# Kernel tuning notes

Measured on AMD Instinct MI355X. Metric: run time of the kernel, lower is better.

## Reference

```python
import jax, jax.numpy as jnp
import numpy as np

SEQ_LEN = 9
HALF = SEQ_LEN // 2  # padding = 4
EPS = 1e-5


def _bn(x, g, b, m, v):
    # BatchNorm1d in eval mode (running stats); dropout disabled (eval).
    return g * (x - m) * jax.lax.rsqrt(v + EPS) + b


def _segment_avgpool(x, segment_key):
    """Per-consecutive-segment AvgPool1d(k=9, stride=1, pad=4, count_include_pad=False).

    x: [B, D] features ordered in time, segment_key: [B] consecutive segment ids.
    Vectorized: windows never cross segment boundaries, so a global prefix sum
    plus per-frame clamped window bounds reproduces the per-segment pooling.
    """
    B, D = x.shape
    idx = jnp.arange(B)
    changed = segment_key[1:] != segment_key[:-1]
    is_start = jnp.concatenate([jnp.array([True]), changed])
    is_end = jnp.concatenate([changed, jnp.array([True])])
    seg_start = jax.lax.cummax(jnp.where(is_start, idx, 0), axis=0)
    seg_end = jax.lax.cummin(jnp.where(is_end, idx, B - 1), axis=0, reverse=True)
    lo = jnp.maximum(idx - HALF, seg_start)
    hi = jnp.minimum(idx + HALF, seg_end)
    csum = jnp.concatenate([jnp.zeros((1, D), x.dtype), jnp.cumsum(x, axis=0)], axis=0)  # [B+1, D]
    sums = csum[hi + 1] - csum[lo]
    counts = (hi - lo + 1).astype(x.dtype)  # count_include_pad=False
    return sums / counts[:, None]


def setup_inputs() -> dict:
    key = jax.random.key(0)
    ks = jax.random.split(key, 16)
    B, F, D3, H = 16384, 2048, 600, 2048
    n_seg = 200
    inp = {
        'img_feat': jax.random.normal(ks[0], (B, F), jnp.float32),
        'segment_key': jnp.sort(jax.random.randint(ks[1], (B,), 0, n_seg, jnp.int32)),
        # to_3d linear
        'W3d': jax.random.normal(ks[2], (D3, F), jnp.float32) * (1.0 / np.sqrt(F)),
        'b3d': jax.random.normal(ks[3], (D3,), jnp.float32) * 0.01,
        # block 1 (bef_pool): Linear(D3->H) + ReLU + BN
        'W1': jax.random.normal(ks[4], (H, D3), jnp.float32) * (1.0 / np.sqrt(D3)),
        'b1': jax.random.normal(ks[5], (H,), jnp.float32) * 0.01,
        'g1': jnp.ones((H,), jnp.float32),
        'be1': jnp.zeros((H,), jnp.float32),
        'm1': jax.random.normal(ks[6], (H,), jnp.float32) * 0.1,
        'v1': jax.random.uniform(ks[7], (H,), jnp.float32, 0.5, 1.5),
        # block 2 (pain head): Linear(H->H) + ReLU + BN
        'W2': jax.random.normal(ks[8], (H, H), jnp.float32) * (1.0 / np.sqrt(H)),
        'b2': jax.random.normal(ks[9], (H,), jnp.float32) * 0.01,
        'g2': jnp.ones((H,), jnp.float32),
        'be2': jnp.zeros((H,), jnp.float32),
        'm2': jax.random.normal(ks[10], (H,), jnp.float32) * 0.1,
        'v2': jax.random.uniform(ks[11], (H,), jnp.float32, 0.5, 1.5),
        # final pain linear H -> 2
        'Wp': jax.random.normal(ks[12], (2, H), jnp.float32) * (1.0 / np.sqrt(H)),
        'bp': jax.random.normal(ks[13], (2,), jnp.float32) * 0.01,
    }
    return inp


def reference(img_feat, segment_key, W3d, b3d, W1, b1, g1, be1, m1, v1,
              W2, b2, g2, be2, m2, v2, Wp, bp):
    latent_3d = img_feat @ W3d.T + b3d                       # [B, D3]
    h = _bn(jax.nn.relu(latent_3d @ W1.T + b1), g1, be1, m1, v1)  # bef_pool, [B, H]
    pooled = _segment_avgpool(h, segment_key)                # ragged windowed avg
    h2 = _bn(jax.nn.relu(pooled @ W2.T + b2), g2, be2, m2, v2)
    output_pain = h2 @ Wp.T + bp                             # [B, 2]
    pain_pred = jax.nn.softmax(output_pain, axis=1)
    return output_pain, pain_pred
```

## Files before the change

kernel.cpp:

```cpp
#include <hip/hip_runtime.h>
#include <hip/hip_bf16.h>
#include <math.h>
#include <stdint.h>

#define DEVI static __device__ __forceinline__

typedef __attribute__((ext_vector_type(8))) short short8;
typedef __attribute__((ext_vector_type(4))) float f32x4;
typedef __attribute__((ext_vector_type(4))) float float4v;
typedef __attribute__((ext_vector_type(4))) unsigned short ushort4v;
typedef __attribute__((ext_vector_type(8))) unsigned short ushort8;

DEVI unsigned short f2bf(float f) {
  unsigned int u = __builtin_bit_cast(unsigned int, f);
  u += 0x7fffu + ((u >> 16) & 1u);
  return (unsigned short)(u >> 16);
}
DEVI float bf2f(unsigned short s) {
  unsigned int u = ((unsigned int)s) << 16;
  return __builtin_bit_cast(float, u);
}

DEVI void gl_lds16(const unsigned short* g, unsigned short* l) {
  __builtin_amdgcn_global_load_lds(
      (const __attribute__((address_space(1))) void*)g,
      (__attribute__((address_space(3))) void*)l, 16, 0, 0);
}

__global__ __launch_bounds__(256) void cast_pad(const float* __restrict__ src,
                                                unsigned short* __restrict__ dst,
                                                int srcR, int srcC, int dstR, int dstC) {
  size_t n4 = (size_t)dstR * (size_t)dstC / 4;
  for (size_t i = (size_t)blockIdx.x * blockDim.x + threadIdx.x; i < n4;
       i += (size_t)gridDim.x * blockDim.x) {
    size_t e = i * 4;
    int r = (int)(e / (size_t)dstC);
    int c = (int)(e % (size_t)dstC);
    float4v v;
    if (r < srcR && c + 3 < srcC) {
      v = *(const float4v*)(src + (size_t)r * srcC + c);
    } else {
#pragma unroll
      for (int j = 0; j < 4; ++j) {
        int cc = c + j;
        v[j] = (r < srcR && cc < srcC) ? src[(size_t)r * srcC + cc] : 0.f;
      }
    }
    ushort4v o;
#pragma unroll
    for (int j = 0; j < 4; ++j) o[j] = f2bf(v[j]);
    *(ushort4v*)(dst + e) = o;
  }
}

#define BARRIER()                                   \
  do {                                              \
    asm volatile("" ::: "memory");                  \
    __builtin_amdgcn_s_barrier();                   \
    asm volatile("" ::: "memory");                  \
  } while (0)
#define LGKM0_SCHED()                                        \
  do {                                                       \
    asm volatile("s_waitcnt lgkmcnt(0)" ::: "memory");       \
    __builtin_amdgcn_sched_barrier(0);                       \
  } while (0)
#define VMCNT(N) asm volatile("s_waitcnt vmcnt(" #N ")" ::: "memory")

#define DSA2(CUR, fmBase)                                                     \
  _Pragma("unroll") for (int i_ = 0; i_ < 4; ++i_)                            \
  _Pragma("unroll") for (int kk_ = 0; kk_ < 2; ++kk_)                         \
      afr[i_][kk_] = *(const short8*)(ldsc + (CUR) * 32768 + aBase[kk_] +     \
                                      ((fmBase) + i_) * 2048);

#define DSB2(CUR, fnBase)                                                     \
  _Pragma("unroll") for (int j_ = 0; j_ < 2; ++j_)                            \
  _Pragma("unroll") for (int kk_ = 0; kk_ < 2; ++kk_)                         \
      bfr[j_][kk_] = *(const short8*)(ldsc + 65536 + (CUR) * 32768 +          \
                                      bBase[kk_] + ((fnBase) + j_) * 2048);

#define MFMAQ(fmB, fnB)                                                       \
  __builtin_amdgcn_s_setprio(1);                                              \
  _Pragma("unroll") for (int i_ = 0; i_ < 4; ++i_)                            \
  _Pragma("unroll") for (int j_ = 0; j_ < 2; ++j_)                            \
  _Pragma("unroll") for (int kk_ = 0; kk_ < 2; ++kk_)                         \
      acc[(fmB) + i_][(fnB) + j_] = __builtin_amdgcn_mfma_f32_16x16x32_bf16(  \
          afr[i_][kk_], bfr[j_][kk_], acc[(fmB) + i_][(fnB) + j_], 0, 0, 0);  \
  __builtin_amdgcn_s_setprio(0);                                              \
  __builtin_amdgcn_sched_barrier(0);

#define STAGE_A(BUF, h, tt)                                                   \
  _Pragma("unroll") for (int j_ = 0; j_ < 2; ++j_)                            \
      gl_lds16(pA + (size_t)((h) * 128 + j_ * 64) * Ks + (size_t)(tt) * 64,   \
               (unsigned short*)(ldsc + (BUF) * 32768 + (h) * 16384 +         \
                                 (j_ * 8 + wid) * 1024));
#define STAGE_B(BUF, h, tt)                                                   \
  _Pragma("unroll") for (int j_ = 0; j_ < 2; ++j_)                            \
      gl_lds16(pB + (size_t)((h) * 128 + j_ * 64) * Ks + (size_t)(tt) * 64,   \
               (unsigned short*)(ldsc + 65536 + (BUF) * 32768 + (h) * 16384 + \
                                 (j_ * 8 + wid) * 1024));

template <int EPI>
__global__ __launch_bounds__(512, 1) void gemm8p(
    const unsigned short* __restrict__ A, const unsigned short* __restrict__ Bt,
    unsigned short* __restrict__ C, int M, int N, int K,
    const float* __restrict__ bias, int biasN,
    const float* __restrict__ g, const float* __restrict__ be,
    const float* __restrict__ mn, const float* __restrict__ vr) {
  extern __shared__ unsigned short lds[];
  char* ldsc = (char*)lds;
  const int tid = threadIdx.x;
  const int wid = tid >> 6;
  const int lane = tid & 63;
  const int wave_m = wid >> 2;
  const int wave_n = wid & 3;
  const int rowA0 = blockIdx.x * 256;
  const int rowB0 = blockIdx.y * 256;
  const int frow = lane & 15;
  const int fk16 = (lane >> 4) * 16;
  const int xorv = (frow & 7) << 4;
  const int NT = K >> 6;
  const size_t Ks = (size_t)K;

  const int arow0 = (wave_m * 128 + frow) * 128;
  const int brow0 = (wave_n * 64 + frow) * 128;
  const int aBase[2] = {arow0 + ((0 + fk16) ^ xorv), arow0 + ((64 + fk16) ^ xorv)};
  const int bBase[2] = {brow0 + ((0 + fk16) ^ xorv), brow0 + ((64 + fk16) ^ xorv)};

  const int srow = tid >> 3;
  const int scolb = (((tid & 7) * 16) ^ (((tid >> 3) & 7) << 4));
  const unsigned short* pA = A + (size_t)(rowA0 + srow) * Ks + (scolb >> 1);
  const unsigned short* pB = Bt + (size_t)(rowB0 + srow) * Ks + (scolb >> 1);

  f32x4 acc[8][4] = {};
  short8 afr[4][2], bfr[2][2];

  STAGE_A(0, 0, 0);
  STAGE_A(0, 1, 0);
  STAGE_B(0, 0, 0);
  STAGE_B(0, 1, 0);
  if (NT > 1) {
    STAGE_A(1, 0, 1);
    STAGE_A(1, 1, 1);
    VMCNT(4);
  } else {
    VMCNT(0);
  }
  BARRIER();

  for (int t = 0; t < NT; t += 2) {
    DSA2(0, 0);
    DSB2(0, 0);
    STAGE_B(1, 0, t + 1);
    BARRIER();
    LGKM0_SCHED();
    MFMAQ(0, 0);
    BARRIER();

    DSB2(0, 2);
    STAGE_B(1, 1, t + 1);
    BARRIER();
    LGKM0_SCHED();
    MFMAQ(0, 2);
    BARRIER();

    DSA2(0, 4);
    BARRIER();
    LGKM0_SCHED();
    MFMAQ(4, 2);
    BARRIER();

    DSB2(0, 0);
    BARRIER();
    if (t + 2 < NT) {
      STAGE_A(0, 0, t + 2);
      STAGE_A(0, 1, t + 2);
      VMCNT(4);
    } else {
      VMCNT(0);
    }
    LGKM0_SCHED();
    MFMAQ(4, 0);
    BARRIER();

    DSA2(1, 0);
    DSB2(1, 0);
    if (t + 2 < NT) STAGE_B(0, 0, t + 2);
    BARRIER();
    LGKM0_SCHED();
    MFMAQ(0, 0);
    BARRIER();

    DSB2(1, 2);
    if (t + 2 < NT) STAGE_B(0, 1, t + 2);
    BARRIER();
    LGKM0_SCHED();
    MFMAQ(0, 2);
    BARRIER();

    DSA2(1, 4);
    BARRIER();
    LGKM0_SCHED();
    MFMAQ(4, 2);
    BARRIER();

    DSB2(1, 0);
    BARRIER();
    if (t + 3 < NT) {
      STAGE_A(1, 0, t + 3);
      STAGE_A(1, 1, t + 3);
      VMCNT(4);
    } else {
      VMCNT(0);
    }
    LGKM0_SCHED();
    MFMAQ(4, 0);
    BARRIER();
  }

  const int rl = (lane >> 4) * 4;
#pragma unroll
  for (int fn = 0; fn < 4; ++fn) {
    int gc = rowB0 + wave_n * 64 + fn * 16 + frow;
    float bb = (gc < biasN) ? bias[gc] : 0.f;
    float gg = 1.f, bbe = 0.f, mm = 0.f, rs = 1.f;
    if (EPI == 1) {
      gg = g[gc];
      bbe = be[gc];
      mm = mn[gc];
      rs = rsqrtf(vr[gc] + 1e-5f);
    }
#pragma unroll
    for (int fm = 0; fm < 8; ++fm) {
      f32x4 v = acc[fm][fn];
#pragma unroll
      for (int r = 0; r < 4; ++r) {
        int gr = rowA0 + wave_m * 128 + fm * 16 + rl + r;
        float x = v[r] + bb;
        if (EPI == 1) {
          x = fmaxf(x, 0.f);
          x = gg * (x - mm) * rs + bbe;
        }
        C[(size_t)gr * N + gc] = f2bf(x);
      }
    }
  }
}

__global__ __launch_bounds__(256) void pool_seg(const unsigned short* __restrict__ h,
                                                const int* __restrict__ key,
                                                unsigned short* __restrict__ pooled,
                                                int B, int D) {
  int row = blockIdx.x;
  int k0 = key[row];
  int down = 0, up = 0;
  while (down < 4 && row - down - 1 >= 0 && key[row - down - 1] == k0) ++down;
  while (up < 4 && row + up + 1 < B && key[row + up + 1] == k0) ++up;
  float inv = 1.f / (float)(down + up + 1);
  int f0 = threadIdx.x * 8;
  float s[8] = {0.f, 0.f, 0.f, 0.f, 0.f, 0.f, 0.f, 0.f};
  for (int dr = -down; dr <= up; ++dr) {
    ushort8 v = *(const ushort8*)(h + (size_t)(row + dr) * D + f0);
#pragma unroll
    for (int j = 0; j < 8; ++j) s[j] += bf2f(v[j]);
  }
  ushort8 o;
#pragma unroll
  for (int j = 0; j < 8; ++j) o[j] = f2bf(s[j] * inv);
  *(ushort8*)(pooled + (size_t)row * D + f0) = o;
}

__global__ __launch_bounds__(256) void final_head(const unsigned short* __restrict__ h2,
                                                  const float* __restrict__ Wp,
                                                  const float* __restrict__ bp,
                                                  float* __restrict__ out, int B, int H) {
  int row = blockIdx.x;
  int f0 = threadIdx.x * 8;
  ushort8 v = *(const ushort8*)(h2 + (size_t)row * H + f0);
  float4v w0a = *(const float4v*)(Wp + f0);
  float4v w0b = *(const float4v*)(Wp + f0 + 4);
  float4v w1a = *(const float4v*)(Wp + H + f0);
  float4v w1b = *(const float4v*)(Wp + H + f0 + 4);
  float a0 = 0.f, a1 = 0.f;
#pragma unroll
  for (int j = 0; j < 4; ++j) {
    float x0 = bf2f(v[j]), x1 = bf2f(v[j + 4]);
    a0 += x0 * w0a[j] + x1 * w0b[j];
    a1 += x0 * w1a[j] + x1 * w1b[j];
  }
#pragma unroll
  for (int off = 32; off > 0; off >>= 1) {
    a0 += __shfl_down(a0, off);
    a1 += __shfl_down(a1, off);
  }
  __shared__ float red[8];
  int wv = threadIdx.x >> 6;
  if ((threadIdx.x & 63) == 0) {
    red[wv] = a0;
    red[4 + wv] = a1;
  }
  __syncthreads();
  if (threadIdx.x == 0) {
    float o0 = red[0] + red[1] + red[2] + red[3] + bp[0];
    float o1 = red[4] + red[5] + red[6] + red[7] + bp[1];
    out[(size_t)row * 2] = o0;
    out[(size_t)row * 2 + 1] = o1;
    float mx = fmaxf(o0, o1);
    float e0 = expf(o0 - mx), e1 = expf(o1 - mx);
    float sden = e0 + e1;
    out[(size_t)B * 2 + (size_t)row * 2] = e0 / sden;
    out[(size_t)B * 2 + (size_t)row * 2 + 1] = e1 / sden;
  }
}

extern "C" void kernel_launch(void* const* d_in, const int* in_sizes, int n_in,
                              void* d_out, int out_size, void* d_ws, size_t ws_size,
                              hipStream_t stream) {
  (void)n_in; (void)out_size; (void)ws_size;
  const float* img = (const float*)d_in[0];
  const int* segkey = (const int*)d_in[1];
  const float* W3d = (const float*)d_in[2];
  const float* b3d = (const float*)d_in[3];
  const float* W1 = (const float*)d_in[4];
  const float* b1 = (const float*)d_in[5];
  const float* g1 = (const float*)d_in[6];
  const float* be1 = (const float*)d_in[7];
  const float* m1 = (const float*)d_in[8];
  const float* v1 = (const float*)d_in[9];
  const float* W2 = (const float*)d_in[10];
  const float* b2 = (const float*)d_in[11];
  const float* g2 = (const float*)d_in[12];
  const float* be2 = (const float*)d_in[13];
  const float* m2 = (const float*)d_in[14];
  const float* v2 = (const float*)d_in[15];
  const float* Wp = (const float*)d_in[16];
  const float* bp = (const float*)d_in[17];

  const int B = in_sizes[1];
  const int F = in_sizes[0] / B;
  const int D3 = in_sizes[3];
  const int H = in_sizes[5];
  const int D3p = 768;

  char* ws = (char*)d_ws;
  size_t off = 0;
  auto alloc = [&](size_t bytes) -> void* {
    void* p = (void*)(ws + off);
    off += (bytes + 255) & ~(size_t)255;
    return p;
  };
  unsigned short* imgb = (unsigned short*)alloc((size_t)B * F * 2);
  unsigned short* W3dp = (unsigned short*)alloc((size_t)D3p * F * 2);
  unsigned short* W1p  = (unsigned short*)alloc((size_t)H * D3p * 2);
  unsigned short* W2b  = (unsigned short*)alloc((size_t)H * H * 2);
  unsigned short* lat  = (unsigned short*)alloc((size_t)B * D3p * 2);
  unsigned short* h    = (unsigned short*)alloc((size_t)B * H * 2);
  unsigned short* pooled = (unsigned short*)alloc((size_t)B * H * 2);
  unsigned short* h2 = imgb;

  float* out = (float*)d_out;

  auto gridFor = [](size_t n4) -> int {
    size_t gsz = (n4 + 255) / 256;
    if (gsz > 4096) gsz = 4096;
    return (int)gsz;
  };

  hipFuncSetAttribute(reinterpret_cast<const void*>(gemm8p<0>),
                      hipFuncAttributeMaxDynamicSharedMemorySize, 131072);
  hipFuncSetAttribute(reinterpret_cast<const void*>(gemm8p<1>),
                      hipFuncAttributeMaxDynamicSharedMemorySize, 131072);

  cast_pad<<<gridFor((size_t)B * F / 4), 256, 0, stream>>>(img, imgb, B, F, B, F);
  cast_pad<<<gridFor((size_t)D3p * F / 4), 256, 0, stream>>>(W3d, W3dp, D3, F, D3p, F);
  cast_pad<<<gridFor((size_t)H * D3p / 4), 256, 0, stream>>>(W1, W1p, H, D3, H, D3p);
  cast_pad<<<gridFor((size_t)H * H / 4), 256, 0, stream>>>(W2, W2b, H, H, H, H);

  dim3 blk(512);
  gemm8p<0><<<dim3(B / 256, D3p / 256), blk, 131072, stream>>>(
      imgb, W3dp, lat, B, D3p, F, b3d, D3, nullptr, nullptr, nullptr, nullptr);
  gemm8p<1><<<dim3(B / 256, H / 256), blk, 131072, stream>>>(
      lat, W1p, h, B, H, D3p, b1, H, g1, be1, m1, v1);
  pool_seg<<<B, H / 8, 0, stream>>>(h, segkey, pooled, B, H);
  gemm8p<1><<<dim3(B / 256, H / 256), blk, 131072, stream>>>(
      pooled, W2b, h2, B, H, H, b2, H, g2, be2, m2, v2);
  final_head<<<B, H / 8, 0, stream>>>(h2, Wp, bp, out, B, H);
}
```

Before: 627.3 us.

## Overlap LDS fragment loads with MFMAs and remap workgroups across XCDs

Each GEMM phase now waits on LDS reads in steps (lgkmcnt 6/4/2/0) and issues the MFMAs for each fragment as soon as its data arrives, instead of draining every LDS read before the MFMA block. The point is to hide LDS latency behind matrix work inside each phase. Separately, the tile index is remapped so that consecutively dispatched workgroups, which round-robin across the 8 XCDs, get contiguous tiles on the same XCD, aiming for better L2 reuse. The risk is that counter-based waits depend on exact instruction ordering, and the remap changes load balance.

```diff
diff --git a/kernel.cpp b/kernel.cpp
--- a/kernel.cpp
+++ b/kernel.cpp
@@ -59,12 +59,13 @@
     __builtin_amdgcn_s_barrier();                   \
     asm volatile("" ::: "memory");                  \
   } while (0)
-#define LGKM0_SCHED()                                        \
+#define VMCNT(N) asm volatile("s_waitcnt vmcnt(" #N ")" ::: "memory")
+#define DS_WAIT(N)                                           \
   do {                                                       \
-    asm volatile("s_waitcnt lgkmcnt(0)" ::: "memory");       \
+    asm volatile("s_waitcnt lgkmcnt(" #N ")" ::: "memory");  \
     __builtin_amdgcn_sched_barrier(0);                       \
   } while (0)
-#define VMCNT(N) asm volatile("s_waitcnt vmcnt(" #N ")" ::: "memory")
+#define SBAR() __builtin_amdgcn_sched_barrier(0)
 
 #define DSA2(CUR, fmBase)                                                     \
   _Pragma("unroll") for (int i_ = 0; i_ < 4; ++i_)                            \
@@ -78,15 +79,17 @@
       bfr[j_][kk_] = *(const short8*)(ldsc + 65536 + (CUR) * 32768 +          \
                                       bBase[kk_] + ((fnBase) + j_) * 2048);
 
-#define MFMAQ(fmB, fnB)                                                       \
-  __builtin_amdgcn_s_setprio(1);                                              \
-  _Pragma("unroll") for (int i_ = 0; i_ < 4; ++i_)                            \
+#define MF_I(FM, FN, AI)                                                      \
   _Pragma("unroll") for (int j_ = 0; j_ < 2; ++j_)                            \
   _Pragma("unroll") for (int kk_ = 0; kk_ < 2; ++kk_)                         \
-      acc[(fmB) + i_][(fnB) + j_] = __builtin_amdgcn_mfma_f32_16x16x32_bf16(  \
-          afr[i_][kk_], bfr[j_][kk_], acc[(fmB) + i_][(fnB) + j_], 0, 0, 0);  \
-  __builtin_amdgcn_s_setprio(0);                                              \
-  __builtin_amdgcn_sched_barrier(0);
+      acc[(FM)][(FN) + j_] = __builtin_amdgcn_mfma_f32_16x16x32_bf16(         \
+          afr[AI][kk_], bfr[j_][kk_], acc[(FM)][(FN) + j_], 0, 0, 0);
+
+#define MF_J(FMB, FN, BJ)                                                     \
+  _Pragma("unroll") for (int i_ = 0; i_ < 4; ++i_)                            \
+  _Pragma("unroll") for (int kk_ = 0; kk_ < 2; ++kk_)                         \
+      acc[(FMB) + i_][(FN)] = __builtin_amdgcn_mfma_f32_16x16x32_bf16(        \
+          afr[i_][kk_], bfr[BJ][kk_], acc[(FMB) + i_][(FN)], 0, 0, 0);
 
 #define STAGE_A(BUF, h, tt)                                                   \
   _Pragma("unroll") for (int j_ = 0; j_ < 2; ++j_)                            \
@@ -98,6 +101,55 @@
       gl_lds16(pB + (size_t)((h) * 128 + j_ * 64) * Ks + (size_t)(tt) * 64,   \
                (unsigned short*)(ldsc + 65536 + (BUF) * 32768 + (h) * 16384 + \
                                  (j_ * 8 + wid) * 1024));
+
+#define PHASE0(CUR, STG)                                                      \
+  DSB2(CUR, 0);                                                               \
+  SBAR();                                                                     \
+  DSA2(CUR, 0);                                                               \
+  STG;                                                                        \
+  BARRIER();                                                                  \
+  __builtin_amdgcn_s_setprio(1);                                              \
+  DS_WAIT(6); MF_I(0, 0, 0);                                                  \
+  DS_WAIT(4); MF_I(1, 0, 1);                                                  \
+  DS_WAIT(2); MF_I(2, 0, 2);                                                  \
+  DS_WAIT(0); MF_I(3, 0, 3);                                                  \
+  __builtin_amdgcn_s_setprio(0);                                              \
+  SBAR();                                                                     \
+  BARRIER();
+
+#define PHASE1(CUR, STG)                                                      \
+  DSB2(CUR, 2);                                                               \
+  STG;                                                                        \
+  BARRIER();                                                                  \
+  __builtin_amdgcn_s_setprio(1);                                              \
+  DS_WAIT(2); MF_J(0, 2, 0);                                                  \
+  DS_WAIT(0); MF_J(0, 3, 1);                                                  \
+  __builtin_amdgcn_s_setprio(0);                                              \
+  SBAR();                                                                     \
+  BARRIER();
+
+#define PHASE2(CUR)                                                           \
+  DSA2(CUR, 4);                                                               \
+  BARRIER();                                                                  \
+  __builtin_amdgcn_s_setprio(1);                                              \
+  DS_WAIT(6); MF_I(4, 2, 0);                                                  \
+  DS_WAIT(4); MF_I(5, 2, 1);                                                  \
+  DS_WAIT(2); MF_I(6, 2, 2);                                                  \
+  DS_WAIT(0); MF_I(7, 2, 3);                                                  \
+  __builtin_amdgcn_s_setprio(0);                                              \
+  SBAR();                                                                     \
+  BARRIER();
+
+#define PHASE3(CUR, STG_AND_VM)                                               \
+  DSB2(CUR, 0);                                                               \
+  BARRIER();                                                                  \
+  STG_AND_VM;                                                                 \
+  __builtin_amdgcn_s_setprio(1);                                              \
+  DS_WAIT(2); MF_J(4, 0, 0);                                                  \
+  DS_WAIT(0); MF_J(4, 1, 1);                                                  \
+  __builtin_amdgcn_s_setprio(0);                                              \
+  SBAR();                                                                     \
+  BARRIER();
 
 template <int EPI>
 __global__ __launch_bounds__(512, 1) void gemm8p(
@@ -113,8 +165,16 @@
   const int lane = tid & 63;
   const int wave_m = wid >> 2;
   const int wave_n = wid & 3;
-  const int rowA0 = blockIdx.x * 256;
-  const int rowB0 = blockIdx.y * 256;
+
+  const int gx = gridDim.x;
+  int flat = blockIdx.x + blockIdx.y * gx;
+  int nwg = gx * gridDim.y;
+  int q = nwg >> 3, r = nwg & 7;
+  int xcd = flat & 7, ofs = flat >> 3;
+  int nf = (xcd < r ? xcd * (q + 1) : r * (q + 1) + (xcd - r) * q) + ofs;
+  const int rowA0 = (nf % gx) * 256;
+  const int rowB0 = (nf / gx) * 256;
+
   const int frow = lane & 15;
   const int fk16 = (lane >> 4) * 16;
   const int xorv = (frow & 7) << 4;
@@ -148,73 +208,27 @@
   BARRIER();
 
   for (int t = 0; t < NT; t += 2) {
-    DSA2(0, 0);
-    DSB2(0, 0);
-    STAGE_B(1, 0, t + 1);
-    BARRIER();
-    LGKM0_SCHED();
-    MFMAQ(0, 0);
-    BARRIER();
-
-    DSB2(0, 2);
-    STAGE_B(1, 1, t + 1);
-    BARRIER();
-    LGKM0_SCHED();
-    MFMAQ(0, 2);
-    BARRIER();
-
-    DSA2(0, 4);
-    BARRIER();
-    LGKM0_SCHED();
-    MFMAQ(4, 2);
-    BARRIER();
-
-    DSB2(0, 0);
-    BARRIER();
+    PHASE0(0, STAGE_B(1, 0, t + 1));
+    PHASE1(0, STAGE_B(1, 1, t + 1));
+    PHASE2(0);
     if (t + 2 < NT) {
-      STAGE_A(0, 0, t + 2);
-      STAGE_A(0, 1, t + 2);
-      VMCNT(4);
+      PHASE3(0, { STAGE_A(0, 0, t + 2); STAGE_A(0, 1, t + 2); VMCNT(4); });
     } else {
-      VMCNT(0);
-    }
-    LGKM0_SCHED();
-    MFMAQ(4, 0);
-    BARRIER();
-
-    DSA2(1, 0);
-    DSB2(1, 0);
-    if (t + 2 < NT) STAGE_B(0, 0, t + 2);
-    BARRIER();
-    LGKM0_SCHED();
-    MFMAQ(0, 0);
-    BARRIER();
-
-    DSB2(1, 2);
-    if (t + 2 < NT) STAGE_B(0, 1, t + 2);
-    BARRIER();
-    LGKM0_SCHED();
-    MFMAQ(0, 2);
-    BARRIER();
-
-    DSA2(1, 4);
-    BARRIER();
-    LGKM0_SCHED();
-    MFMAQ(4, 2);
-    BARRIER();
-
-    DSB2(1, 0);
-    BARRIER();
+      PHASE3(0, { VMCNT(0); });
+    }
+    if (t + 2 < NT) {
+      PHASE0(1, STAGE_B(0, 0, t + 2));
+      PHASE1(1, STAGE_B(0, 1, t + 2));
+    } else {
+      PHASE0(1, {});
+      PHASE1(1, {});
+    }
+    PHASE2(1);
     if (t + 3 < NT) {
-      STAGE_A(1, 0, t + 3);
-      STAGE_A(1, 1, t + 3);
-      VMCNT(4);
+      PHASE3(1, { STAGE_A(1, 0, t + 3); STAGE_A(1, 1, t + 3); VMCNT(4); });
     } else {
-      VMCNT(0);
-    }
-    LGKM0_SCHED();
-    MFMAQ(4, 0);
-    BARRIER();
+      PHASE3(1, { VMCNT(0); });
+    }
   }
 
   const int rl = (lane >> 4) * 4;
@@ -233,9 +247,9 @@
     for (int fm = 0; fm < 8; ++fm) {
       f32x4 v = acc[fm][fn];
 #pragma unroll
-      for (int r = 0; r < 4; ++r) {
-        int gr = rowA0 + wave_m * 128 + fm * 16 + rl + r;
-        float x = v[r] + bb;
+      for (int r2 = 0; r2 < 4; ++r2) {
+        int gr = rowA0 + wave_m * 128 + fm * 16 + rl + r2;
+        float x = v[r2] + bb;
         if (EPI == 1) {
           x = fmaxf(x, 0.f);
           x = gg * (x - mm) * rs + bbe;
```

Result: slower. 1.026 ms (+63.6%).
